# Performance work log

Measured on AMD Instinct MI355X. Metric: run time of the kernel, lower is better.

## Reference

```python
import jax, jax.numpy as jnp
import numpy as np

B = 16384
N_DENSE = 13
N_TABLES = 26
V = 1000000
E = 2  # embedding dim (hard-coded in source)


def setup_inputs() -> dict:
    key = jax.random.key(0)
    ks = jax.random.split(key, 12)
    x_dense = jax.random.normal(ks[0], (B, N_DENSE), dtype=jnp.float32)
    x_cat = jax.random.randint(ks[1], (B, N_TABLES), 0, V, dtype=jnp.int64)
    # All tables share the same num_embeddings, so stack into one [T, V, E] array.
    emb = jax.random.normal(ks[2], (N_TABLES, V, E), dtype=jnp.float32) * 0.05
    # bottom MLP: 13 -> 3 -> 2
    bot_w1 = jax.random.normal(ks[3], (N_DENSE, 3), dtype=jnp.float32) * 0.1
    bot_b1 = jnp.zeros((3,), dtype=jnp.float32)
    bot_w2 = jax.random.normal(ks[4], (3, 2), dtype=jnp.float32) * 0.1
    bot_b2 = jnp.zeros((2,), dtype=jnp.float32)
    # top MLP: 54 -> 4 -> 2 -> 1
    top_w1 = jax.random.normal(ks[5], (E * N_TABLES + 2, 4), dtype=jnp.float32) * 0.1
    top_b1 = jnp.zeros((4,), dtype=jnp.float32)
    top_w2 = jax.random.normal(ks[6], (4, 2), dtype=jnp.float32) * 0.1
    top_b2 = jnp.zeros((2,), dtype=jnp.float32)
    top_w3 = jax.random.normal(ks[7], (2, 1), dtype=jnp.float32) * 0.1
    top_b3 = jnp.zeros((1,), dtype=jnp.float32)
    return {
        "x_dense": x_dense, "x_cat": x_cat, "emb": emb,
        "bot_w1": bot_w1, "bot_b1": bot_b1, "bot_w2": bot_w2, "bot_b2": bot_b2,
        "top_w1": top_w1, "top_b1": top_b1, "top_w2": top_w2, "top_b2": top_b2,
        "top_w3": top_w3, "top_b3": top_b3,
    }


def reference(x_dense, x_cat, emb, bot_w1, bot_b1, bot_w2, bot_b2,
              top_w1, top_b1, top_w2, top_b2, top_w3, top_b3):
    # bottom MLP on dense features: [B,13] -> [B,2]
    d = jax.nn.relu(x_dense @ bot_w1 + bot_b1)
    d = jax.nn.relu(d @ bot_w2 + bot_b2)
    # multi-table embedding gather: emb[t, x_cat[:, t]] -> [B, T, E]
    table_idx = jnp.arange(N_TABLES)[None, :]  # [1, T]
    e = emb[table_idx, x_cat]                  # [B, T, E]
    e = e.reshape(e.shape[0], N_TABLES * E)    # [B, 52]
    x = jnp.concatenate([d, e], axis=1)        # [B, 54]
    # top MLP: 54 -> 4 -> 2 -> 1 with sigmoid
    h = jax.nn.relu(x @ top_w1 + top_b1)
    h = jax.nn.relu(h @ top_w2 + top_b2)
    out = jax.nn.sigmoid(h @ top_w3 + top_b3)
    return out
```

## Files before the change

### kernel.cpp

```cpp
#include <hip/hip_runtime.h>
#include <math.h>

#define B_TOTAL   16384
#define N_DENSE   13
#define N_TABLES  26
#define V_ROWS    1000000
#define E_DIM     2

__global__ __launch_bounds__(64) void dlrm_fused_kernel(
    const float* __restrict__ x_dense,
    const int*   __restrict__ x_cat,
    const float* __restrict__ emb,
    const float* __restrict__ bw1,
    const float* __restrict__ bb1,
    const float* __restrict__ bw2,
    const float* __restrict__ bb2,
    const float* __restrict__ tw1,
    const float* __restrict__ tb1,
    const float* __restrict__ tw2,
    const float* __restrict__ tb2,
    const float* __restrict__ tw3,
    const float* __restrict__ tb3,
    float*       __restrict__ out)
{
    const int b = blockIdx.x * blockDim.x + threadIdx.x;
    if (b >= B_TOTAL) return;

    float ev[2 * N_TABLES];
    {
        const long long cbase = (long long)b * N_TABLES;
        #pragma unroll
        for (int t = 0; t < N_TABLES; ++t) {
            const int idx = x_cat[cbase + t];
            const float2 v = *reinterpret_cast<const float2*>(
                emb + ((size_t)t * V_ROWS + (size_t)idx) * E_DIM);
            ev[2 * t]     = v.x;
            ev[2 * t + 1] = v.y;
        }
    }

    float xd[N_DENSE];
    {
        const long long dbase = (long long)b * N_DENSE;
        #pragma unroll
        for (int i = 0; i < N_DENSE; ++i) xd[i] = x_dense[dbase + i];
    }
    float d1[3];
    #pragma unroll
    for (int j = 0; j < 3; ++j) {
        float acc = bb1[j];
        #pragma unroll
        for (int i = 0; i < N_DENSE; ++i) acc = fmaf(xd[i], bw1[i * 3 + j], acc);
        d1[j] = fmaxf(acc, 0.0f);
    }
    float d2[2];
    #pragma unroll
    for (int j = 0; j < 2; ++j) {
        float acc = bb2[j];
        #pragma unroll
        for (int i = 0; i < 3; ++i) acc = fmaf(d1[i], bw2[i * 2 + j], acc);
        d2[j] = fmaxf(acc, 0.0f);
    }

    float h1[4];
    #pragma unroll
    for (int j = 0; j < 4; ++j) {
        float acc = tb1[j];
        acc = fmaf(d2[0], tw1[0 * 4 + j], acc);
        acc = fmaf(d2[1], tw1[1 * 4 + j], acc);
        #pragma unroll
        for (int i = 0; i < 2 * N_TABLES; ++i)
            acc = fmaf(ev[i], tw1[(2 + i) * 4 + j], acc);
        h1[j] = fmaxf(acc, 0.0f);
    }
    float h2[2];
    #pragma unroll
    for (int j = 0; j < 2; ++j) {
        float acc = tb2[j];
        #pragma unroll
        for (int i = 0; i < 4; ++i) acc = fmaf(h1[i], tw2[i * 2 + j], acc);
        h2[j] = fmaxf(acc, 0.0f);
    }
    float z = tb3[0];
    z = fmaf(h2[0], tw3[0], z);
    z = fmaf(h2[1], tw3[1], z);

    out[b] = 1.0f / (1.0f + expf(-z));
}

extern "C" void kernel_launch(void* const* d_in, const int* in_sizes, int n_in,
                              void* d_out, int out_size, void* d_ws, size_t ws_size,
                              hipStream_t stream) {
    const float* x_dense = (const float*)d_in[0];
    const int*   x_cat   = (const int*)  d_in[1];
    const float* emb     = (const float*)d_in[2];
    const float* bw1     = (const float*)d_in[3];
    const float* bb1     = (const float*)d_in[4];
    const float* bw2     = (const float*)d_in[5];
    const float* bb2     = (const float*)d_in[6];
    const float* tw1     = (const float*)d_in[7];
    const float* tb1     = (const float*)d_in[8];
    const float* tw2     = (const float*)d_in[9];
    const float* tb2     = (const float*)d_in[10];
    const float* tw3     = (const float*)d_in[11];
    const float* tb3     = (const float*)d_in[12];
    float* out = (float*)d_out;

    const int block = 64;
    const int grid  = (B_TOTAL + block - 1) / block;
    dlrm_fused_kernel<<<grid, block, 0, stream>>>(
        x_dense, x_cat, emb, bw1, bb1, bw2, bb2,
        tw1, tb1, tw2, tb2, tw3, tb3, out);
}
```

Baseline: 271.5 us.

## Split each sample's embedding gather across 8 lanes with shuffle reduction

Each batch row is now handled by 8 threads. Each thread gathers 3-4 embedding rows and computes a partial top-layer-1 dot product, and the partials are summed with xor shuffles. This is meant to raise memory-level parallelism and occupancy for the random gathers and to coalesce the x_cat index reads. Block size goes from 64 to 256. The dense bottom MLP is now computed redundantly by all 8 lanes, and only lane 0 writes the output.

```diff
diff --git a/kernel.cpp b/kernel.cpp
--- a/kernel.cpp
+++ b/kernel.cpp
@@ -5,9 +5,9 @@
 #define N_DENSE   13
 #define N_TABLES  26
 #define V_ROWS    1000000
-#define E_DIM     2
+#define SPLIT     8
 
-__global__ __launch_bounds__(64) void dlrm_fused_kernel(
+__global__ __launch_bounds__(256) void dlrm_fused_kernel(
     const float* __restrict__ x_dense,
     const int*   __restrict__ x_cat,
     const float* __restrict__ emb,
@@ -23,69 +23,98 @@
     const float* __restrict__ tb3,
     float*       __restrict__ out)
 {
-    const int b = blockIdx.x * blockDim.x + threadIdx.x;
+    const int gid = blockIdx.x * blockDim.x + threadIdx.x;
+    const int b   = gid >> 3;
+    const int sub = gid & (SPLIT - 1);
     if (b >= B_TOTAL) return;
 
-    float ev[2 * N_TABLES];
-    {
-        const long long cbase = (long long)b * N_TABLES;
-        #pragma unroll
-        for (int t = 0; t < N_TABLES; ++t) {
-            const int idx = x_cat[cbase + t];
-            const float2 v = *reinterpret_cast<const float2*>(
-                emb + ((size_t)t * V_ROWS + (size_t)idx) * E_DIM);
-            ev[2 * t]     = v.x;
-            ev[2 * t + 1] = v.y;
+    const int cbase = b * N_TABLES;
+
+    int idx0 = x_cat[cbase + sub];
+    int idx1 = x_cat[cbase + sub + 8];
+    int idx2 = x_cat[cbase + sub + 16];
+    int idx3 = 0;
+    const bool has3 = (sub + 24) < N_TABLES;
+    if (has3) idx3 = x_cat[cbase + sub + 24];
+
+    const float2 e0 = *reinterpret_cast<const float2*>(
+        emb + ((size_t)(sub)      * V_ROWS + (size_t)idx0) * 2);
+    const float2 e1 = *reinterpret_cast<const float2*>(
+        emb + ((size_t)(sub + 8)  * V_ROWS + (size_t)idx1) * 2);
+    const float2 e2 = *reinterpret_cast<const float2*>(
+        emb + ((size_t)(sub + 16) * V_ROWS + (size_t)idx2) * 2);
+    float2 e3 = make_float2(0.0f, 0.0f);
+    if (has3) e3 = *reinterpret_cast<const float2*>(
+        emb + ((size_t)(sub + 24) * V_ROWS + (size_t)idx3) * 2);
+
+    float acc[4];
+    #pragma unroll
+    for (int j = 0; j < 4; ++j) {
+        float a = 0.0f;
+        a = fmaf(e0.x, tw1[(2 + 2 * sub)          * 4 + j], a);
+        a = fmaf(e0.y, tw1[(3 + 2 * sub)          * 4 + j], a);
+        a = fmaf(e1.x, tw1[(2 + 2 * (sub + 8))    * 4 + j], a);
+        a = fmaf(e1.y, tw1[(3 + 2 * (sub + 8))    * 4 + j], a);
+        a = fmaf(e2.x, tw1[(2 + 2 * (sub + 16))   * 4 + j], a);
+        a = fmaf(e2.y, tw1[(3 + 2 * (sub + 16))   * 4 + j], a);
+        if (has3) {
+            a = fmaf(e3.x, tw1[(2 + 2 * (sub + 24)) * 4 + j], a);
+            a = fmaf(e3.y, tw1[(3 + 2 * (sub + 24)) * 4 + j], a);
         }
+        acc[j] = a;
+    }
+
+    #pragma unroll
+    for (int j = 0; j < 4; ++j) {
+        acc[j] += __shfl_xor(acc[j], 1);
+        acc[j] += __shfl_xor(acc[j], 2);
+        acc[j] += __shfl_xor(acc[j], 4);
     }
 
     float xd[N_DENSE];
     {
-        const long long dbase = (long long)b * N_DENSE;
+        const int dbase = b * N_DENSE;
         #pragma unroll
         for (int i = 0; i < N_DENSE; ++i) xd[i] = x_dense[dbase + i];
     }
     float d1[3];
     #pragma unroll
     for (int j = 0; j < 3; ++j) {
-        float acc = bb1[j];
+        float a = bb1[j];
         #pragma unroll
-        for (int i = 0; i < N_DENSE; ++i) acc = fmaf(xd[i], bw1[i * 3 + j], acc);
-        d1[j] = fmaxf(acc, 0.0f);
+        for (int i = 0; i < N_DENSE; ++i) a = fmaf(xd[i], bw1[i * 3 + j], a);
+        d1[j] = fmaxf(a, 0.0f);
     }
     float d2[2];
     #pragma unroll
     for (int j = 0; j < 2; ++j) {
-        float acc = bb2[j];
+        float a = bb2[j];
         #pragma unroll
-        for (int i = 0; i < 3; ++i) acc = fmaf(d1[i], bw2[i * 2 + j], acc);
-        d2[j] = fmaxf(acc, 0.0f);
+        for (int i = 0; i < 3; ++i) a = fmaf(d1[i], bw2[i * 2 + j], a);
+        d2[j] = fmaxf(a, 0.0f);
     }
 
     float h1[4];
     #pragma unroll
     for (int j = 0; j < 4; ++j) {
-        float acc = tb1[j];
-        acc = fmaf(d2[0], tw1[0 * 4 + j], acc);
-        acc = fmaf(d2[1], tw1[1 * 4 + j], acc);
-        #pragma unroll
-        for (int i = 0; i < 2 * N_TABLES; ++i)
-            acc = fmaf(ev[i], tw1[(2 + i) * 4 + j], acc);
-        h1[j] = fmaxf(acc, 0.0f);
+        float a = acc[j] + tb1[j];
+        a = fmaf(d2[0], tw1[0 * 4 + j], a);
+        a = fmaf(d2[1], tw1[1 * 4 + j], a);
+        h1[j] = fmaxf(a, 0.0f);
     }
     float h2[2];
     #pragma unroll
     for (int j = 0; j < 2; ++j) {
-        float acc = tb2[j];
+        float a = tb2[j];
         #pragma unroll
-        for (int i = 0; i < 4; ++i) acc = fmaf(h1[i], tw2[i * 2 + j], acc);
-        h2[j] = fmaxf(acc, 0.0f);
+        for (int i = 0; i < 4; ++i) a = fmaf(h1[i], tw2[i * 2 + j], a);
+        h2[j] = fmaxf(a, 0.0f);
     }
     float z = tb3[0];
     z = fmaf(h2[0], tw3[0], z);
     z = fmaf(h2[1], tw3[1], z);
 
-    out[b] = 1.0f / (1.0f + expf(-z));
+    if (sub == 0) out[b] = 1.0f / (1.0f + expf(-z));
 }
 
 extern "C" void kernel_launch(void* const* d_in, const int* in_sizes, int n_in,
@@ -106,8 +135,9 @@
     const float* tb3     = (const float*)d_in[12];
     float* out = (float*)d_out;
 
-    const int block = 64;
-    const int grid  = (B_TOTAL + block - 1) / block;
+    const int threads = B_TOTAL * SPLIT;
+    const int block   = 256;
+    const int grid    = threads / block;
     dlrm_fused_kernel<<<grid, block, 0, stream>>>(
         x_dense, x_cat, emb, bw1, bb1, bw2, bb2,
         tw1, tb1, tw2, tb2, tw3, tb3, out);
```

After: 276.8 us. About the same (+2.0%).
